# Performance work log

Measured on AMD Instinct MI355X. Metric: run time of the kernel, lower is better.

The kernel has to match this reference:

```python
import jax, jax.numpy as jnp
import numpy as np

N = 65536      # nodes
E = 1048576    # edges (avg degree 16)
B = 64         # graphs in batch
H = 128        # hidden
L = 3          # message-passing layers
MAXZ = 100


def _segment_mean(x, idx, n):
    s = jax.ops.segment_sum(x, idx, num_segments=n)
    c = jax.ops.segment_sum(jnp.ones((idx.shape[0], 1), x.dtype), idx, num_segments=n)
    return s / jnp.maximum(c, 1.0)


def setup_inputs() -> dict:
    key = jax.random.key(0)
    ks = jax.random.split(key, 24)
    w = lambda k, shape: jax.random.normal(k, shape, dtype=jnp.float32) * 0.05
    inp = {
        "pos": jax.random.normal(ks[0], (N, 3), dtype=jnp.float32),
        "z": jax.random.randint(ks[1], (N,), 0, MAXZ),
        "batch": jnp.sort(jax.random.randint(ks[2], (N,), 0, B)),
        "edge_index": jax.random.randint(ks[3], (2, E), 0, N),
        "node_type": jax.random.randint(ks[4], (N,), 0, 2),
        # parameters (weights stored [in, out] so y = x @ W + b)
        "emb": w(ks[5], (MAXZ, H)),
        "lin_in_w": w(ks[6], (H + 3, H)),
        "lin_in_b": jnp.zeros((H,), jnp.float32),
        "msg_w1": w(ks[7], (L, 2 * H + 1, H)),
        "msg_b1": jnp.zeros((L, H), jnp.float32),
        "msg_w2": w(ks[8], (L, H, H)),
        "msg_b2": jnp.zeros((L, H), jnp.float32),
        "upd_w": w(ks[9], (L, 2 * H, H)),
        "upd_b": jnp.zeros((L, H), jnp.float32),
        "ro_w1": w(ks[10], (H, H)),
        "ro_b1": jnp.zeros((H,), jnp.float32),
        "ro_w2": w(ks[11], (H, 1)),
        "ro_b2": jnp.zeros((1,), jnp.float32),
    }
    return inp


def reference(pos, z, batch, edge_index, node_type,
              emb, lin_in_w, lin_in_b,
              msg_w1, msg_b1, msg_w2, msg_b2,
              upd_w, upd_b, ro_w1, ro_b1, ro_w2, ro_b2):
    # centroid-centered positions per graph
    center = _segment_mean(pos, batch, B)           # [B,3]
    pos_rel = pos - center[batch]                   # [N,3]

    x = jnp.concatenate([emb[z], pos_rel], axis=-1) @ lin_in_w + lin_in_b  # [N,H]

    row, col = edge_index[0], edge_index[1]
    rel = pos_rel[col] - pos_rel[row]               # [E,3]
    dist = jnp.linalg.norm(rel, axis=-1, keepdims=True)  # [E,1]

    for l in range(L):
        m_in = jnp.concatenate([x[col], x[row], dist], axis=-1)      # [E,2H+1]
        h = jax.nn.relu(m_in @ msg_w1[l] + msg_b1[l])
        m_ij = jax.nn.relu(h @ msg_w2[l] + msg_b2[l])                # [E,H] (dropout=identity, eval)
        m_i = _segment_mean(m_ij, row, N)                            # [N,H]
        x = jax.nn.relu(jnp.concatenate([x, m_i], axis=-1) @ upd_w[l] + upd_b[l])

    lig_mask = (node_type == 1).astype(x.dtype)                      # [N]
    lig_counts = jnp.maximum(jax.ops.segment_sum(lig_mask, batch, num_segments=B), 1.0)
    g = jax.ops.segment_sum(x * lig_mask[:, None], batch, num_segments=B)  # [B,H]
    g = g / lig_counts[:, None]

    hg = jax.nn.relu(g @ ro_w1 + ro_b1)
    affinity = (hg @ ro_w2 + ro_b2).squeeze(-1)                      # [B]
    return affinity
```

## Files before the change

kernel.cpp:

```cpp
#include <hip/hip_runtime.h>
#include <hip/hip_bf16.h>
#include <hip/hip_fp16.h>
#include <math.h>

#define NN 65536
#define NE 1048576
#define NB 64
#define HD 128
#define NL 3

#define O_CSUM   0
#define O_CCNT   192
#define O_LCNT   256
#define O_GSUM   320
#define O_DEGI   8512
#define O_POSREL 74048
#define O_RC     270656
#define O_XHI    1319232
#define O_XLO    5513536
#define O_P      9707840
#define O_DIST   13902144
#define O_Q      18096448
#define O_C1H    22290752
#define O_EW     22291456
#define O_MSUM   26485056
#define O_W2T    34873664
#define O_W1TH   34898240
#define O_W1TL   34947392
#define O_WUTH   34996544
#define O_WUTL   35045696
#define O_CHK    35094848

typedef __attribute__((ext_vector_type(8))) short bf16x8;
typedef __attribute__((ext_vector_type(8))) _Float16 f16x8;
typedef __attribute__((ext_vector_type(8))) unsigned short u16x8;
typedef __attribute__((ext_vector_type(4))) float f32x4;

__device__ __forceinline__ void atomAdd(float* p, float v) { unsafeAtomicAdd(p, v); }

__device__ __forceinline__ unsigned short f2bf(float f) {
    union { __hip_bfloat16 h; unsigned short u; } cv;
    cv.h = __float2bfloat16(f);
    return cv.u;
}
__device__ __forceinline__ float bf2f(unsigned short u) {
    union { float f; unsigned v; } c; c.v = ((unsigned)u) << 16; return c.f;
}
__device__ __forceinline__ void split2(float v, unsigned short& h, unsigned short& l) {
    h = f2bf(v); l = f2bf(v - bf2f(h));
}
__device__ __forceinline__ unsigned short f2h(float f) {
    union { __half h; unsigned short u; } c; c.h = __float2half(f); return c.u;
}

__global__ __launch_bounds__(256) void stats_kernel(
    const float* __restrict__ pos, const int* __restrict__ batch,
    const int* __restrict__ ntype,
    float* __restrict__ csum, float* __restrict__ ccnt, float* __restrict__ lcnt)
{
    __shared__ float s[NB * 5];
    const int tid = threadIdx.x;
    for (int i = tid; i < NB * 5; i += 256) s[i] = 0.f;
    __syncthreads();
    const int n = blockIdx.x * 256 + tid;
    const int b = batch[n];
    atomicAdd(&s[b*5+0], pos[n*3+0]);
    atomicAdd(&s[b*5+1], pos[n*3+1]);
    atomicAdd(&s[b*5+2], pos[n*3+2]);
    atomicAdd(&s[b*5+3], 1.f);
    if (ntype[n] == 1) atomicAdd(&s[b*5+4], 1.f);
    __syncthreads();
    for (int i = tid; i < NB * 5; i += 256) {
        float v = s[i];
        if (v != 0.f) {
            int b2 = i / 5, f = i - b2*5;
            if (f < 3)       atomAdd(&csum[b2*3+f], v);
            else if (f == 3) atomAdd(&ccnt[b2], v);
            else             atomAdd(&lcnt[b2], v);
        }
    }
}

__global__ __launch_bounds__(256) void deg_kernel(const int* __restrict__ row, int* __restrict__ degi)
{
    const int e = blockIdx.x * 256 + threadIdx.x;
    atomicAdd(&degi[row[e]], 1);
}

__global__ __launch_bounds__(256) void scanA_kernel(const int* __restrict__ degi, int* __restrict__ chunkSum)
{
    __shared__ int red[4];
    const int t = threadIdx.x, b = blockIdx.x;
    int v = degi[b*256 + t];
    #pragma unroll
    for (int off = 32; off > 0; off >>= 1) v += __shfl_down(v, off, 64);
    if ((t & 63) == 0) red[t >> 6] = v;
    __syncthreads();
    if (t == 0) chunkSum[b] = red[0] + red[1] + red[2] + red[3];
}

__global__ __launch_bounds__(256) void scanB_kernel(int* __restrict__ chunkSum)
{
    __shared__ int s[256];
    const int t = threadIdx.x;
    const int v = chunkSum[t];
    s[t] = v;
    __syncthreads();
    #pragma unroll
    for (int off = 1; off < 256; off <<= 1) {
        int u = (t >= off) ? s[t - off] : 0;
        __syncthreads();
        s[t] += u;
        __syncthreads();
    }
    chunkSum[t] = s[t] - v;
}

__global__ __launch_bounds__(256) void scanC_kernel(const int* __restrict__ degi,
                                                    const int* __restrict__ chunkOff,
                                                    int* __restrict__ rowStart)
{
    __shared__ int s[256];
    const int t = threadIdx.x, b = blockIdx.x;
    const int v = degi[b*256 + t];
    s[t] = v;
    __syncthreads();
    #pragma unroll
    for (int off = 1; off < 256; off <<= 1) {
        int u = (t >= off) ? s[t - off] : 0;
        __syncthreads();
        s[t] += u;
        __syncthreads();
    }
    rowStart[b*256 + t] = chunkOff[b] + s[t] - v;
}

__global__ __launch_bounds__(256) void scatter_kernel(
    const int* __restrict__ row, const int* __restrict__ col,
    const int* __restrict__ rowStart, int* __restrict__ cnt,
    unsigned int* __restrict__ rcS,
    const float* __restrict__ posrel, float* __restrict__ distS)
{
    const int e = blockIdx.x * 256 + threadIdx.x;
    const int r = row[e], c = col[e];
    const float dx = posrel[c*3+0] - posrel[r*3+0];
    const float dy = posrel[c*3+1] - posrel[r*3+1];
    const float dz = posrel[c*3+2] - posrel[r*3+2];
    const int p = rowStart[r] + atomicAdd(&cnt[r], 1);
    rcS[p] = ((unsigned)r << 16) | (unsigned)c;
    distS[p] = sqrtf(dx*dx + dy*dy + dz*dz);
}

__global__ __launch_bounds__(256) void posrel_kernel(
    const float* __restrict__ pos, const int* __restrict__ batch,
    const float* __restrict__ csum, const float* __restrict__ ccnt,
    float* __restrict__ posrel)
{
    const int n = blockIdx.x * 256 + threadIdx.x;
    const int b = batch[n];
    const float inv = 1.f / fmaxf(ccnt[b], 1.f);
    posrel[n*3+0] = pos[n*3+0] - csum[b*3+0]*inv;
    posrel[n*3+1] = pos[n*3+1] - csum[b*3+1]*inv;
    posrel[n*3+2] = pos[n*3+2] - csum[b*3+2]*inv;
}

__global__ __launch_bounds__(256) void wprep_kernel(
    const float* __restrict__ mw1, const float* __restrict__ uw,
    const float* __restrict__ mw2,
    const float* __restrict__ lin_w, const float* __restrict__ lin_b,
    const float* __restrict__ emb,
    unsigned short* __restrict__ w1th, unsigned short* __restrict__ w1tl,
    unsigned short* __restrict__ wuth, unsigned short* __restrict__ wutl,
    unsigned short* __restrict__ w2t, unsigned short* __restrict__ c1h,
    float* __restrict__ EW)
{
    const int idx = blockIdx.x * 256 + threadIdx.x;
    {
        const int l = idx >> 15, rem = idx & 32767;
        const int w = rem & 7, t = rem >> 3;
        const int c = t & 255, kb = t >> 8;
        const int k = kb*8 + w;
        const int kk = (c < 128) ? k : (128 + k);
        const int cc = c & 127;
        const float v = mw1[l*257*128 + kk*128 + cc];
        unsigned short h, lo; split2(v, h, lo);
        w1th[idx] = h; w1tl[idx] = lo;
    }
    {
        const int l = idx >> 15, rem = idx & 32767;
        const int w = rem & 7, t = rem >> 3;
        const int c = t & 127, kb = t >> 7;
        const int k = kb*8 + w;
        const float v = uw[l*256*128 + k*128 + c];
        unsigned short h, lo; split2(v, h, lo);
        wuth[idx] = h; wutl[idx] = lo;
    }
    if (idx < 49152) {
        const int l = idx >> 14, rem = idx & 16383;
        const int blk = rem >> 3, win = rem & 7;
        const int n = blk >> 4, cs = blk & 15;
        const int c = cs ^ (n & 7);
        const int k = c*8 + win;
        w2t[idx] = f2h(mw2[(l << 14) + k*128 + n]);
    }
    if (idx < 384) {
        const int l = idx >> 7, c = idx & 127;
        c1h[idx] = f2h(mw1[l*257*128 + 256*128 + c]);
    }
    if (idx < 12800) {
        const int j = idx & 127, zz = idx >> 7;
        float acc = lin_b[j];
        for (int k = 0; k < 128; ++k)
            acc += emb[zz*128 + k] * lin_w[k*128 + j];
        EW[idx] = acc;
    }
}

__global__ __launch_bounds__(256) void lin_in_kernel(
    const float* __restrict__ EW, const float* __restrict__ posrel,
    const int* __restrict__ zidx, const float* __restrict__ lin_w,
    unsigned short* __restrict__ xhi, unsigned short* __restrict__ xlo)
{
    const int tid = threadIdx.x;
    const int node = blockIdx.x * 16 + (tid >> 4);
    const int j0 = (tid & 15) * 8;

    const int zz = zidx[node];
    const float px = posrel[node*3+0], py = posrel[node*3+1], pz = posrel[node*3+2];

    const float4 e0 = *(const float4*)&EW[zz*128 + j0];
    const float4 e1 = *(const float4*)&EW[zz*128 + j0 + 4];
    const float4 wx0 = *(const float4*)&lin_w[128*128 + j0];
    const float4 wx1 = *(const float4*)&lin_w[128*128 + j0 + 4];
    const float4 wy0 = *(const float4*)&lin_w[129*128 + j0];
    const float4 wy1 = *(const float4*)&lin_w[129*128 + j0 + 4];
    const float4 wz0 = *(const float4*)&lin_w[130*128 + j0];
    const float4 wz1 = *(const float4*)&lin_w[130*128 + j0 + 4];

    float o[8];
    o[0] = e0.x + px*wx0.x + py*wy0.x + pz*wz0.x;
    o[1] = e0.y + px*wx0.y + py*wy0.y + pz*wz0.y;
    o[2] = e0.z + px*wx0.z + py*wy0.z + pz*wz0.z;
    o[3] = e0.w + px*wx0.w + py*wy0.w + pz*wz0.w;
    o[4] = e1.x + px*wx1.x + py*wy1.x + pz*wz1.x;
    o[5] = e1.y + px*wx1.y + py*wy1.y + pz*wz1.y;
    o[6] = e1.z + px*wx1.z + py*wy1.z + pz*wz1.z;
    o[7] = e1.w + px*wx1.w + py*wy1.w + pz*wz1.w;

    ushort4 h0, l0, h1, l1;
    split2(o[0], h0.x, l0.x); split2(o[1], h0.y, l0.y);
    split2(o[2], h0.z, l0.z); split2(o[3], h0.w, l0.w);
    split2(o[4], h1.x, l1.x); split2(o[5], h1.y, l1.y);
    split2(o[6], h1.z, l1.z); split2(o[7], h1.w, l1.w);
    *(ushort4*)&xhi[node*HD + j0]     = h0;
    *(ushort4*)&xhi[node*HD + j0 + 4] = h1;
    *(ushort4*)&xlo[node*HD + j0]     = l0;
    *(ushort4*)&xlo[node*HD + j0 + 4] = l1;
}

__global__ __launch_bounds__(256) void pq_gemm(
    const unsigned short* __restrict__ xhi, const unsigned short* __restrict__ xlo,
    const unsigned short* __restrict__ w1th, const unsigned short* __restrict__ w1tl,
    unsigned short* __restrict__ Ph, unsigned short* __restrict__ Qh,
    float* __restrict__ msum, const float* __restrict__ b1)
{
    const int tid = threadIdx.x;
    const int l = tid & 63, w = tid >> 6;
    const int mr = l & 15, qd = l >> 4;
    const int n0 = blockIdx.x * 64;
    const int c0 = w * 64;

    {
        float4* mz = (float4*)&msum[(long)blockIdx.x * 8192];
        const float4 z4 = make_float4(0.f, 0.f, 0.f, 0.f);
        #pragma unroll
        for (int it = 0; it < 8; ++it) mz[tid + it*256] = z4;
    }

    f32x4 acc[4][4];
    #pragma unroll
    for (int mt = 0; mt < 4; ++mt)
        #pragma unroll
        for (int nt = 0; nt < 4; ++nt) acc[mt][nt] = (f32x4){0.f,0.f,0.f,0.f};

    #pragma unroll
    for (int ks = 0; ks < 4; ++ks) {
        const int kof = ks*32 + qd*8;
        const int kb  = ks*4 + qd;
        bf16x8 ah[4], al[4], bh[4], bl[4];
        #pragma unroll
        for (int mt = 0; mt < 4; ++mt) {
            const int node = n0 + mt*16 + mr;
            ah[mt] = *(const bf16x8*)&xhi[node*HD + kof];
            al[mt] = *(const bf16x8*)&xlo[node*HD + kof];
        }
        #pragma unroll
        for (int nt = 0; nt < 4; ++nt) {
            const int c = c0 + nt*16 + mr;
            bh[nt] = *(const bf16x8*)&w1th[(kb << 11) + (c << 3)];
            bl[nt] = *(const bf16x8*)&w1tl[(kb << 11) + (c << 3)];
        }
        #pragma unroll
        for (int mt = 0; mt < 4; ++mt)
            #pragma unroll
            for (int nt = 0; nt < 4; ++nt) {
                acc[mt][nt] = __builtin_amdgcn_mfma_f32_16x16x32_bf16(ah[mt], bh[nt], acc[mt][nt], 0,0,0);
                acc[mt][nt] = __builtin_amdgcn_mfma_f32_16x16x32_bf16(ah[mt], bl[nt], acc[mt][nt], 0,0,0);
                acc[mt][nt] = __builtin_amdgcn_mfma_f32_16x16x32_bf16(al[mt], bh[nt], acc[mt][nt], 0,0,0);
            }
    }

    unsigned short* __restrict__ dst = (w < 2) ? Ph : Qh;
    const int cbase = (w < 2) ? c0 : c0 - 128;
    #pragma unroll
    for (int mt = 0; mt < 4; ++mt)
        #pragma unroll
        for (int nt = 0; nt < 4; ++nt) {
            const int cc = cbase + nt*16 + mr;
            const float bb = (w < 2) ? 0.f : b1[cc];
            #pragma unroll
            for (int r = 0; r < 4; ++r) {
                const int node = n0 + mt*16 + qd*4 + r;
                dst[(long)node*HD + cc] = f2h(acc[mt][nt][r] + bb);
            }
        }
}

__global__ __launch_bounds__(256) void upd_gemm(
    unsigned short* __restrict__ xhi, unsigned short* __restrict__ xlo,
    const float* __restrict__ msum, const int* __restrict__ degi,
    const unsigned short* __restrict__ wuth, const unsigned short* __restrict__ wutl,
    const float* __restrict__ bias)
{
    const int tid = threadIdx.x;
    const int l = tid & 63, w = tid >> 6;
    const int mr = l & 15, qd = l >> 4;
    const int n0 = blockIdx.x * 64 + w*16;
    const int node = n0 + mr;
    const float inv = 1.f / fmaxf((float)degi[node], 1.f);

    f32x4 acc[8];
    #pragma unroll
    for (int nt = 0; nt < 8; ++nt) acc[nt] = (f32x4){0.f,0.f,0.f,0.f};

    #pragma unroll 1
    for (int ks = 0; ks < 8; ++ks) {
        const int kof = ks*32 + qd*8;
        const int kb  = ks*4 + qd;
        bf16x8 ah, al;
        if (ks < 4) {
            ah = *(const bf16x8*)&xhi[node*HD + kof];
            al = *(const bf16x8*)&xlo[node*HD + kof];
        } else {
            const int mk = kof - 128;
            const float4 v0 = *(const float4*)&msum[(long)node*HD + mk];
            const float4 v1 = *(const float4*)&msum[(long)node*HD + mk + 4];
            union { bf16x8 v; unsigned short u[8]; } hh, ll;
            float vv[8] = { v0.x*inv, v0.y*inv, v0.z*inv, v0.w*inv,
                            v1.x*inv, v1.y*inv, v1.z*inv, v1.w*inv };
            #pragma unroll
            for (int i = 0; i < 8; ++i) split2(vv[i], hh.u[i], ll.u[i]);
            ah = hh.v; al = ll.v;
        }
        #pragma unroll
        for (int nt = 0; nt < 8; ++nt) {
            const int c = nt*16 + mr;
            const bf16x8 bh = *(const bf16x8*)&wuth[(kb << 10) + (c << 3)];
            const bf16x8 bl = *(const bf16x8*)&wutl[(kb << 10) + (c << 3)];
            acc[nt] = __builtin_amdgcn_mfma_f32_16x16x32_bf16(ah, bh, acc[nt], 0,0,0);
            acc[nt] = __builtin_amdgcn_mfma_f32_16x16x32_bf16(ah, bl, acc[nt], 0,0,0);
            acc[nt] = __builtin_amdgcn_mfma_f32_16x16x32_bf16(al, bh, acc[nt], 0,0,0);
        }
    }

    #pragma unroll
    for (int nt = 0; nt < 8; ++nt) {
        const int c = nt*16 + mr;
        const float bb = bias[c];
        #pragma unroll
        for (int r = 0; r < 4; ++r) {
            const int nd = n0 + qd*4 + r;
            const float o = fmaxf(acc[nt][r] + bb, 0.f);
            unsigned short h, lo; split2(o, h, lo);
            xhi[nd*HD + c] = h;
            xlo[nd*HD + c] = lo;
        }
    }
}

__global__ __launch_bounds__(256) void edge_msg_kernel(
    const unsigned short* __restrict__ Ph, const unsigned short* __restrict__ Qh,
    const float* __restrict__ distS,
    const unsigned int* __restrict__ rcS,
    const unsigned short* __restrict__ c1h,
    const unsigned short* __restrict__ w2t,
    const float* __restrict__ b2,
    float* __restrict__ msum)
{
    __shared__ __align__(16) unsigned short w2s[16384];
    const int tid = threadIdx.x;

    {
        const uint4* __restrict__ src = (const uint4*)w2t;
        uint4* dst = (uint4*)w2s;
        #pragma unroll
        for (int i = 0; i < 8; ++i) dst[tid + i*256] = src[tid + i*256];
    }

    const long e0 = (long)blockIdx.x * 256;
    const int l  = tid & 63;
    const int w  = tid >> 6;
    const int mr = l & 15;
    const int qd = l >> 4;
    const long ebase = e0 + w*64;

    const int aoff = ((mr >> 2) << 4) + (mr & 3);
    int ecol[4], erow[4];
    #pragma unroll
    for (int m = 0; m < 4; ++m) {
        const unsigned rc = rcS[ebase + aoff + m*4];
        erow[m] = (int)(rc >> 16); ecol[m] = (int)(rc & 0xffffu);
    }

    u16x8 praw[4][4];
    #pragma unroll
    for (int m = 0; m < 4; ++m)
        #pragma unroll
        for (int kk = 0; kk < 4; ++kk)
            praw[m][kk] = *(const u16x8*)&Ph[(long)ecol[m]*HD + kk*32 + qd*8];

    float edist[4];
    #pragma unroll
    for (int m = 0; m < 4; ++m) edist[m] = distS[ebase + aoff + m*4];

    unsigned rcv[16];
    {
        const uint4* rc4 = (const uint4*)&rcS[ebase + qd*16];
        #pragma unroll
        for (int i = 0; i < 4; ++i) {
            const uint4 v = rc4[i];
            rcv[i*4+0] = (v.x >> 16) << 7; rcv[i*4+1] = (v.y >> 16) << 7;
            rcv[i*4+2] = (v.z >> 16) << 7; rcv[i*4+3] = (v.w >> 16) << 7;
        }
    }
    unsigned m1 = 0;
    #pragma unroll
    for (int i = 1; i < 16; ++i) if (rcv[i] == rcv[i-1]) m1 |= (1u << i);
    const unsigned m2 = m1 & (m1 << 1);
    const unsigned m4 = m2 & (m2 << 2);
    const unsigned m8 = m4 & (m4 << 4);

    float b2v[8];
    #pragma unroll
    for (int t = 0; t < 8; ++t) b2v[t] = b2[t*16 + mr];

    f16x8 c8[4];
    #pragma unroll
    for (int kk = 0; kk < 4; ++kk) {
        union { u16x8 raw; f16x8 v; } cu;
        cu.raw = ((const u16x8*)c1h)[kk*4 + qd];
        c8[kk] = cu.v;
    }

    const f16x8 z8 = {};
    f16x8 afr[4][4];
    #pragma unroll
    for (int m = 0; m < 4; ++m) {
        union { u16x8 raw; f16x8 v; } qu[4];
        #pragma unroll
        for (int kk = 0; kk < 4; ++kk)
            qu[kk].raw = *(const u16x8*)&Qh[(long)erow[m]*HD + kk*32 + qd*8];
        const _Float16 d16 = (_Float16)edist[m];
        #pragma unroll
        for (int kk = 0; kk < 4; ++kk) {
            union { u16x8 raw; f16x8 v; } pu; pu.raw = praw[m][kk];
            f16x8 s = pu.v + qu[kk].v + d16 * c8[kk];
            afr[m][kk] = __builtin_elementwise_max(s, z8);
        }
    }

    __syncthreads();

    #pragma unroll 1
    for (int t = 0; t < 8; ++t) {
        f16x8 bfr[4];
        #pragma unroll
        for (int kk = 0; kk < 4; ++kk) {
            const int c = kk*4 + qd;
            const int blk = (t*16 + mr)*16 + (c ^ (mr & 7));
            union { u16x8 raw; f16x8 v; } bu;
            bu.raw = *(const u16x8*)&w2s[blk*8];
            bfr[kk] = bu.v;
        }
        const int colg = t*16 + mr;
        const float bb = b2v[t];

        f32x4 acc[4];
        #pragma unroll
        for (int m = 0; m < 4; ++m) acc[m] = (f32x4){0.f, 0.f, 0.f, 0.f};
        __builtin_amdgcn_s_setprio(1);
        #pragma unroll
        for (int kk = 0; kk < 4; ++kk)
            #pragma unroll
            for (int m = 0; m < 4; ++m)
                acc[m] = __builtin_amdgcn_mfma_f32_16x16x32_f16(afr[m][kk], bfr[kk], acc[m], 0, 0, 0);
        __builtin_amdgcn_s_setprio(0);

        float v[16];
        #pragma unroll
        for (int i = 0; i < 16; ++i) v[i] = fmaxf(acc[i>>2][i&3] + bb, 0.f);
        #pragma unroll
        for (int i = 15; i >= 1; --i) if (m1 & (1u << i)) v[i] += v[i-1];
        #pragma unroll
        for (int i = 15; i >= 2; --i) if (m2 & (1u << i)) v[i] += v[i-2];
        #pragma unroll
        for (int i = 15; i >= 4; --i) if (m4 & (1u << i)) v[i] += v[i-4];
        #pragma unroll
        for (int i = 15; i >= 8; --i) if (m8 & (1u << i)) v[i] += v[i-8];
        #pragma unroll
        for (int i = 0; i < 16; ++i)
            if (!(m1 & (2u << i)))
                atomAdd(&msum[(long)(rcv[i] + colg)], v[i]);
    }
}

__global__ __launch_bounds__(256) void gsum_kernel(
    const unsigned short* __restrict__ xhi, const unsigned short* __restrict__ xlo,
    const int* __restrict__ batch,
    const int* __restrict__ ntype, float* __restrict__ gsum)
{
    const int tid = threadIdx.x;
    const int cg = tid & 31;
    const int ns = tid >> 5;
    const int n0 = blockIdx.x * 512 + ns * 64;

    int bprev = -1;
    float4 run = make_float4(0.f, 0.f, 0.f, 0.f);
    for (int i = 0; i < 64; ++i) {
        const int n = n0 + i;
        if (ntype[n] != 1) continue;
        const int b = batch[n];
        const ushort4 h  = *(const ushort4*)&xhi[(long)n*HD + cg*4];
        const ushort4 lo = *(const ushort4*)&xlo[(long)n*HD + cg*4];
        float4 v;
        v.x = bf2f(h.x) + bf2f(lo.x);
        v.y = bf2f(h.y) + bf2f(lo.y);
        v.z = bf2f(h.z) + bf2f(lo.z);
        v.w = bf2f(h.w) + bf2f(lo.w);
        if (b != bprev) {
            if (bprev >= 0) {
                float* dst = &gsum[bprev*HD + cg*4];
                atomAdd(dst+0, run.x); atomAdd(dst+1, run.y);
                atomAdd(dst+2, run.z); atomAdd(dst+3, run.w);
            }
            bprev = b; run = v;
        } else {
            run.x += v.x; run.y += v.y; run.z += v.z; run.w += v.w;
        }
    }
    if (bprev >= 0) {
        float* dst = &gsum[bprev*HD + cg*4];
        atomAdd(dst+0, run.x); atomAdd(dst+1, run.y);
        atomAdd(dst+2, run.z); atomAdd(dst+3, run.w);
    }
}

__global__ __launch_bounds__(128) void readout_kernel(
    const float* __restrict__ gsum, const float* __restrict__ lcnt,
    const float* __restrict__ w1, const float* __restrict__ b1,
    const float* __restrict__ w2, const float* __restrict__ b2,
    float* __restrict__ out)
{
    __shared__ float gs[HD];
    __shared__ float red[2];
    const int b = blockIdx.x, j = threadIdx.x;
    gs[j] = gsum[b*HD + j] / fmaxf(lcnt[b], 1.f);
    __syncthreads();
    float acc = b1[j];
    for (int k = 0; k < HD; ++k) acc += gs[k]*w1[k*HD + j];
    float hg = fmaxf(acc, 0.f) * w2[j];
    #pragma unroll
    for (int off = 32; off > 0; off >>= 1) hg += __shfl_down(hg, off, 64);
    if ((j & 63) == 0) red[j >> 6] = hg;
    __syncthreads();
    if (j == 0) out[b] = red[0] + red[1] + b2[0];
}

extern "C" void kernel_launch(void* const* d_in, const int* in_sizes, int n_in,
                              void* d_out, int out_size, void* d_ws, size_t ws_size,
                              hipStream_t stream)
{
    const float* pos   = (const float*)d_in[0];
    const int*   z     = (const int*)d_in[1];
    const int*   batch = (const int*)d_in[2];
    const int*   eidx  = (const int*)d_in[3];
    const int*   ntype = (const int*)d_in[4];
    const float* emb   = (const float*)d_in[5];
    const float* lin_w = (const float*)d_in[6];
    const float* lin_b = (const float*)d_in[7];
    const float* mw1   = (const float*)d_in[8];
    const float* mb1   = (const float*)d_in[9];
    const float* mw2   = (const float*)d_in[10];
    const float* mb2   = (const float*)d_in[11];
    const float* uw    = (const float*)d_in[12];
    const float* ub    = (const float*)d_in[13];
    const float* rw1   = (const float*)d_in[14];
    const float* rb1   = (const float*)d_in[15];
    const float* rw2   = (const float*)d_in[16];
    const float* rb2   = (const float*)d_in[17];

    const int* row = eidx;
    const int* col = eidx + NE;

    float* ws     = (float*)d_ws;
    float* csum   = ws + O_CSUM;
    float* ccnt   = ws + O_CCNT;
    float* lcnt   = ws + O_LCNT;
    float* gsum   = ws + O_GSUM;
    int*   degi   = (int*)(ws + O_DEGI);
    float* posrel = ws + O_POSREL;
    unsigned int* rcS = (unsigned int*)(ws + O_RC);
    unsigned short* xhi = (unsigned short*)(ws + O_XHI);
    unsigned short* xlo = (unsigned short*)(ws + O_XLO);
    unsigned short* Ph  = (unsigned short*)(ws + O_P);
    float* distS  = ws + O_DIST;
    unsigned short* Qh  = (unsigned short*)(ws + O_Q);
    unsigned short* c1h = (unsigned short*)(ws + O_C1H);
    float* EW     = ws + O_EW;
    float* msum   = ws + O_MSUM;
    unsigned short* w2t  = (unsigned short*)(ws + O_W2T);
    unsigned short* w1th = (unsigned short*)(ws + O_W1TH);
    unsigned short* w1tl = (unsigned short*)(ws + O_W1TL);
    unsigned short* wuth = (unsigned short*)(ws + O_WUTH);
    unsigned short* wutl = (unsigned short*)(ws + O_WUTL);
    int* chunkSum = (int*)(ws + O_CHK);
    int* rowStart = (int*)xhi;
    int* cnt      = (int*)xhi + NN;

    (void)hipMemsetAsync(ws, 0, (size_t)(O_DEGI + NN) * sizeof(float), stream);
    (void)hipMemsetAsync(cnt, 0, (size_t)NN * sizeof(int), stream);

    stats_kernel  <<<NN/256, 256, 0, stream>>>(pos, batch, ntype, csum, ccnt, lcnt);
    deg_kernel    <<<NE/256, 256, 0, stream>>>(row, degi);
    posrel_kernel <<<NN/256, 256, 0, stream>>>(pos, batch, csum, ccnt, posrel);
    scanA_kernel  <<<256, 256, 0, stream>>>(degi, chunkSum);
    scanB_kernel  <<<1, 256, 0, stream>>>(chunkSum);
    scanC_kernel  <<<256, 256, 0, stream>>>(degi, chunkSum, rowStart);
    scatter_kernel<<<NE/256, 256, 0, stream>>>(row, col, rowStart, cnt, rcS, posrel, distS);
    wprep_kernel  <<<384, 256, 0, stream>>>(mw1, uw, mw2, lin_w, lin_b, emb,
                                            w1th, w1tl, wuth, wutl, w2t, c1h, EW);

    lin_in_kernel<<<NN/16, 256, 0, stream>>>(EW, posrel, z, lin_w, xhi, xlo);

    for (int l = 0; l < NL; ++l) {
        pq_gemm<<<NN/64, 256, 0, stream>>>(xhi, xlo,
                                           w1th + (size_t)l*32768, w1tl + (size_t)l*32768,
                                           Ph, Qh, msum, mb1 + (size_t)l*HD);
        edge_msg_kernel<<<NE/256, 256, 0, stream>>>(Ph, Qh, distS, rcS,
                                                    c1h + (size_t)l*HD,
                                                    w2t + (size_t)l*16384, mb2 + l*HD, msum);
        upd_gemm<<<NN/64, 256, 0, stream>>>(xhi, xlo, msum, degi,
                                            wuth + (size_t)l*32768, wutl + (size_t)l*32768,
                                            ub + l*HD);
    }

    gsum_kernel   <<<NN/512, 256, 0, stream>>>(xhi, xlo, batch, ntype, gsum);
    readout_kernel<<<NB, 128, 0, stream>>>(gsum, lcnt, rw1, rb1, rw2, rb2, (float*)d_out);
}
```

Measured before the change: 789.8 us.

## Swap MFMA operands for row-contiguous vector stores; simplify edge segmented sum

In the node GEMM and the update GEMM, the A and B operands of the MFMA are swapped. Each lane then holds four consecutive output columns of one node, so the epilogue writes ushort4 vectors and loads the bias as float4, replacing scattered 2-byte stores. In the edge message kernel, the log-step segmented scan over 16 edges becomes a sequential running sum keyed on a same-row mask, and the s_setprio hints around the MFMAs are dropped. The sequential scan has a serial dependency chain but fewer instructions, and removing setprio may change wave scheduling.

```diff
diff --git a/kernel.cpp b/kernel.cpp
--- a/kernel.cpp
+++ b/kernel.cpp
@@ -304,26 +304,30 @@
         for (int mt = 0; mt < 4; ++mt)
             #pragma unroll
             for (int nt = 0; nt < 4; ++nt) {
-                acc[mt][nt] = __builtin_amdgcn_mfma_f32_16x16x32_bf16(ah[mt], bh[nt], acc[mt][nt], 0,0,0);
-                acc[mt][nt] = __builtin_amdgcn_mfma_f32_16x16x32_bf16(ah[mt], bl[nt], acc[mt][nt], 0,0,0);
-                acc[mt][nt] = __builtin_amdgcn_mfma_f32_16x16x32_bf16(al[mt], bh[nt], acc[mt][nt], 0,0,0);
+                acc[mt][nt] = __builtin_amdgcn_mfma_f32_16x16x32_bf16(bh[nt], ah[mt], acc[mt][nt], 0,0,0);
+                acc[mt][nt] = __builtin_amdgcn_mfma_f32_16x16x32_bf16(bl[nt], ah[mt], acc[mt][nt], 0,0,0);
+                acc[mt][nt] = __builtin_amdgcn_mfma_f32_16x16x32_bf16(bh[nt], al[mt], acc[mt][nt], 0,0,0);
             }
     }
 
     unsigned short* __restrict__ dst = (w < 2) ? Ph : Qh;
     const int cbase = (w < 2) ? c0 : c0 - 128;
     #pragma unroll
-    for (int mt = 0; mt < 4; ++mt)
+    for (int mt = 0; mt < 4; ++mt) {
+        const int node = n0 + mt*16 + mr;
         #pragma unroll
         for (int nt = 0; nt < 4; ++nt) {
-            const int cc = cbase + nt*16 + mr;
-            const float bb = (w < 2) ? 0.f : b1[cc];
-            #pragma unroll
-            for (int r = 0; r < 4; ++r) {
-                const int node = n0 + mt*16 + qd*4 + r;
-                dst[(long)node*HD + cc] = f2h(acc[mt][nt][r] + bb);
-            }
-        }
+            const int ccb = cbase + nt*16 + qd*4;
+            float4 bb4 = make_float4(0.f, 0.f, 0.f, 0.f);
+            if (w >= 2) bb4 = *(const float4*)&b1[ccb];
+            ushort4 o4;
+            o4.x = f2h(acc[mt][nt][0] + bb4.x);
+            o4.y = f2h(acc[mt][nt][1] + bb4.y);
+            o4.z = f2h(acc[mt][nt][2] + bb4.z);
+            o4.w = f2h(acc[mt][nt][3] + bb4.w);
+            *(ushort4*)&dst[(long)node*HD + ccb] = o4;
+        }
+    }
 }
 
 __global__ __launch_bounds__(256) void upd_gemm(
@@ -367,24 +371,25 @@
             const int c = nt*16 + mr;
             const bf16x8 bh = *(const bf16x8*)&wuth[(kb << 10) + (c << 3)];
             const bf16x8 bl = *(const bf16x8*)&wutl[(kb << 10) + (c << 3)];
-            acc[nt] = __builtin_amdgcn_mfma_f32_16x16x32_bf16(ah, bh, acc[nt], 0,0,0);
-            acc[nt] = __builtin_amdgcn_mfma_f32_16x16x32_bf16(ah, bl, acc[nt], 0,0,0);
-            acc[nt] = __builtin_amdgcn_mfma_f32_16x16x32_bf16(al, bh, acc[nt], 0,0,0);
+            acc[nt] = __builtin_amdgcn_mfma_f32_16x16x32_bf16(bh, ah, acc[nt], 0,0,0);
+            acc[nt] = __builtin_amdgcn_mfma_f32_16x16x32_bf16(bl, ah, acc[nt], 0,0,0);
+            acc[nt] = __builtin_amdgcn_mfma_f32_16x16x32_bf16(bh, al, acc[nt], 0,0,0);
         }
     }
 
     #pragma unroll
     for (int nt = 0; nt < 8; ++nt) {
-        const int c = nt*16 + mr;
-        const float bb = bias[c];
-        #pragma unroll
-        for (int r = 0; r < 4; ++r) {
-            const int nd = n0 + qd*4 + r;
-            const float o = fmaxf(acc[nt][r] + bb, 0.f);
-            unsigned short h, lo; split2(o, h, lo);
-            xhi[nd*HD + c] = h;
-            xlo[nd*HD + c] = lo;
-        }
+        const int cb = nt*16 + qd*4;
+        const float4 bb4 = *(const float4*)&bias[cb];
+        float o0 = fmaxf(acc[nt][0] + bb4.x, 0.f);
+        float o1 = fmaxf(acc[nt][1] + bb4.y, 0.f);
+        float o2 = fmaxf(acc[nt][2] + bb4.z, 0.f);
+        float o3 = fmaxf(acc[nt][3] + bb4.w, 0.f);
+        ushort4 h4, l4;
+        split2(o0, h4.x, l4.x); split2(o1, h4.y, l4.y);
+        split2(o2, h4.z, l4.z); split2(o3, h4.w, l4.w);
+        *(ushort4*)&xhi[(long)node*HD + cb] = h4;
+        *(ushort4*)&xlo[(long)node*HD + cb] = l4;
     }
 }
 
@@ -443,12 +448,9 @@
             rcv[i*4+2] = (v.z >> 16) << 7; rcv[i*4+3] = (v.w >> 16) << 7;
         }
     }
-    unsigned m1 = 0;
-    #pragma unroll
-    for (int i = 1; i < 16; ++i) if (rcv[i] == rcv[i-1]) m1 |= (1u << i);
-    const unsigned m2 = m1 & (m1 << 1);
-    const unsigned m4 = m2 & (m2 << 2);
-    const unsigned m8 = m4 & (m4 << 4);
+    unsigned sameMask = 0;
+    #pragma unroll
+    for (int i = 1; i < 16; ++i) if (rcv[i] == rcv[i-1]) sameMask |= (1u << i);
 
     float b2v[8];
     #pragma unroll
@@ -498,29 +500,20 @@
         f32x4 acc[4];
         #pragma unroll
         for (int m = 0; m < 4; ++m) acc[m] = (f32x4){0.f, 0.f, 0.f, 0.f};
-        __builtin_amdgcn_s_setprio(1);
         #pragma unroll
         for (int kk = 0; kk < 4; ++kk)
             #pragma unroll
             for (int m = 0; m < 4; ++m)
                 acc[m] = __builtin_amdgcn_mfma_f32_16x16x32_f16(afr[m][kk], bfr[kk], acc[m], 0, 0, 0);
-        __builtin_amdgcn_s_setprio(0);
-
-        float v[16];
-        #pragma unroll
-        for (int i = 0; i < 16; ++i) v[i] = fmaxf(acc[i>>2][i&3] + bb, 0.f);
-        #pragma unroll
-        for (int i = 15; i >= 1; --i) if (m1 & (1u << i)) v[i] += v[i-1];
-        #pragma unroll
-        for (int i = 15; i >= 2; --i) if (m2 & (1u << i)) v[i] += v[i-2];
-        #pragma unroll
-        for (int i = 15; i >= 4; --i) if (m4 & (1u << i)) v[i] += v[i-4];
-        #pragma unroll
-        for (int i = 15; i >= 8; --i) if (m8 & (1u << i)) v[i] += v[i-8];
-        #pragma unroll
-        for (int i = 0; i < 16; ++i)
-            if (!(m1 & (2u << i)))
-                atomAdd(&msum[(long)(rcv[i] + colg)], v[i]);
+
+        float run = 0.f;
+        #pragma unroll
+        for (int i = 0; i < 16; ++i) {
+            const float v = fmaxf(acc[i>>2][i&3] + bb, 0.f);
+            run = (sameMask & (1u << i)) ? run + v : v;
+            if (!(sameMask & (2u << i)))
+                atomAdd(&msum[(long)(rcv[i] + colg)], run);
+        }
     }
 }
 
```

Result: faster. 772.6 us (-2.2%).
